# Performance work log

Hardware: AMD Instinct MI355X
Metric: run time of the kernel (lower is better)

Reference implementation:

```python
import jax, jax.numpy as jnp
import numpy as np

B, N, H, D, E = 32, 1000, 256, 128, 512000
NB = B * N


def setup_inputs() -> dict:
    key = jax.random.key(0)
    ks = jax.random.split(key, 16)
    s = 0.05
    inp = {
        "x": jax.random.normal(ks[0], (B, D), jnp.float32),
        "h_prev": jax.random.normal(ks[1], (B, N, H), jnp.float32),
        "c_prev": jax.random.normal(ks[2], (B, N, H), jnp.float32),
        "src": jax.random.randint(ks[3], (E,), 0, NB, jnp.int32),
        "dst": jax.random.randint(ks[4], (E,), 0, NB, jnp.int32),
        "Wi": jax.random.normal(ks[5], (D, H), jnp.float32) * s,
        "bi": jax.random.normal(ks[6], (H,), jnp.float32) * s,
        "Wf": jax.random.normal(ks[7], (D, H), jnp.float32) * s,
        "bf": jax.random.normal(ks[8], (H,), jnp.float32) * s,
        "Wo": jax.random.normal(ks[9], (D, H), jnp.float32) * s,
        "bo": jax.random.normal(ks[10], (H,), jnp.float32) * s,
        "Wc": jax.random.normal(ks[11], (D, H), jnp.float32) * s,
        "bc": jax.random.normal(ks[12], (H,), jnp.float32) * s,
        "Wg": jax.random.normal(ks[13], (H, H), jnp.float32) * s,
        "bg": jax.random.normal(ks[14], (H,), jnp.float32) * s,
    }
    return inp


def _graph_conv(src, dst, h, Wg, bg):
    # DGL GraphConv, norm='both': D_dst^{-1/2} * sum_edges (D_src^{-1/2} * h_src) @ W + b
    nb = h.shape[0]
    ones = jnp.ones(src.shape[0], h.dtype)
    deg_out = jnp.maximum(jax.ops.segment_sum(ones, src, num_segments=nb), 1.0)
    deg_in = jnp.maximum(jax.ops.segment_sum(ones, dst, num_segments=nb), 1.0)
    h = h * (deg_out ** -0.5)[:, None]          # pre-normalize by src out-degree
    agg = jax.ops.segment_sum(h[src], dst, num_segments=nb)  # irregular gather/scatter
    agg = agg * (deg_in ** -0.5)[:, None]       # post-normalize by dst in-degree
    return agg @ Wg + bg


def reference(x, h_prev, c_prev, src, dst, Wi, bi, Wf, bf, Wo, bo, Wc, bc, Wg, bg):
    b, n, hh = h_prev.shape
    h_conv = _graph_conv(src, dst, h_prev.reshape(b * n, hh), Wg, bg).reshape(b, n, hh)
    # four input-gate projections, broadcast over nodes
    xi = (x @ Wi + bi)[:, None, :]
    xf = (x @ Wf + bf)[:, None, :]
    xo = (x @ Wo + bo)[:, None, :]
    xc = (x @ Wc + bc)[:, None, :]
    i_t = jax.nn.sigmoid(xi + h_conv)
    f_t = jax.nn.sigmoid(xf + h_conv)
    o_t = jax.nn.sigmoid(xo + h_conv)
    c_tilde = jnp.tanh(xc + h_conv)
    c_t = f_t * c_prev + i_t * c_tilde
    h_t = o_t * jnp.tanh(c_t)
    return h_t, c_t
```

## Files before the change

### kernel.cpp

```cpp
#include <hip/hip_runtime.h>

#define BB 32
#define NN 1000
#define HH 256
#define DD 128
#define EE 512000
#define NB (BB * NN)
#define PADLOG 6
#define PAD (1 << PADLOG)

#define DEGO_OFF 0
#define DEGI_OFF (NB)
#define GATE_OFF (2 * NB)
#define WGB_OFF (GATE_OFF + 4 * BB * HH)
#define PADC_OFF (WGB_OFF + (HH * HH) / 2)
#define HW_OFF (PADC_OFF + NB * PAD)

using bf16x8 = __attribute__((ext_vector_type(8))) short;
using f32x4 = __attribute__((ext_vector_type(4))) float;

__device__ inline unsigned short f2bf(float x) {
    unsigned u = __float_as_uint(x);
    return (unsigned short)((u + 0x7FFFu + ((u >> 16) & 1u)) >> 16);
}
__device__ inline float bf2f(unsigned short u) {
    return __uint_as_float(((unsigned)u) << 16);
}

__global__ __launch_bounds__(256) void k_fatA(
    const int* __restrict__ src, const int* __restrict__ dst,
    int* __restrict__ deg_out, int* __restrict__ deg_in,
    int* __restrict__ padded, const float* __restrict__ Wg,
    unsigned short* __restrict__ wgb, const float* __restrict__ x,
    const float* __restrict__ Wi, const float* __restrict__ bi,
    const float* __restrict__ Wf, const float* __restrict__ bf_,
    const float* __restrict__ Wo, const float* __restrict__ bo,
    const float* __restrict__ Wc, const float* __restrict__ bc,
    float* __restrict__ gates) {
    int blk = blockIdx.x;
    int t = threadIdx.x;
    if (blk < BB) {
        __shared__ float xs[DD];
        int b = blk;
        if (t < DD) xs[t] = x[b * DD + t];
        __syncthreads();
        float ai = bi[t], af = bf_[t], ao = bo[t], ac = bc[t];
#pragma unroll 4
        for (int k = 0; k < DD; k++) {
            float xv = xs[k];
            ai += xv * Wi[k * HH + t];
            af += xv * Wf[k * HH + t];
            ao += xv * Wo[k * HH + t];
            ac += xv * Wc[k * HH + t];
        }
        gates[0 * BB * HH + b * HH + t] = ai;
        gates[1 * BB * HH + b * HH + t] = af;
        gates[2 * BB * HH + b * HH + t] = ao;
        gates[3 * BB * HH + b * HH + t] = ac;
    } else if (blk < BB + 256) {
        int o = (blk - BB) * 256 + t;
        int j = o & 7;
        int c = o >> 3;
        int lane = c & 63;
        int nt = (c >> 6) & 15;
        int kk = c >> 10;
        int k = kk * 32 + (lane >> 4) * 8 + j;
        int n = nt * 16 + (lane & 15);
        wgb[o] = f2bf(Wg[k * HH + n]);
    } else {
        int e = (blk - (BB + 256)) * 256 + t;
        int s = src[e];
        int d = dst[e];
        atomicAdd(&deg_out[s], 1);
        int p = atomicAdd(&deg_in[d], 1);
        if (p < PAD) padded[(d << PADLOG) + p] = s;
    }
}

__global__ __launch_bounds__(256) void k_fatC(
    const int* __restrict__ deg_out, const float* __restrict__ h,
    const unsigned short* __restrict__ wgb, unsigned short* __restrict__ hw) {
    int blk = blockIdx.x;
    int t = threadIdx.x;
    int lane = t & 63;
    int w = t >> 6;
    int quad = lane >> 4;
    int mrow = lane & 15;
    int r0 = blk * 64 + w * 16;
    int row = r0 + mrow;
    float sc = rsqrtf((float)max(deg_out[row], 1));

    f32x4 acc[16];
#pragma unroll
    for (int nt = 0; nt < 16; nt++) acc[nt] = (f32x4){0.f, 0.f, 0.f, 0.f};

#pragma unroll 1
    for (int kk = 0; kk < 8; kk++) {
        const float* ap = h + (size_t)row * HH + kk * 32 + quad * 8;
        float4 a0 = *(const float4*)ap;
        float4 a1 = *(const float4*)(ap + 4);
        bf16x8 af;
        af[0] = (short)f2bf(a0.x * sc);
        af[1] = (short)f2bf(a0.y * sc);
        af[2] = (short)f2bf(a0.z * sc);
        af[3] = (short)f2bf(a0.w * sc);
        af[4] = (short)f2bf(a1.x * sc);
        af[5] = (short)f2bf(a1.y * sc);
        af[6] = (short)f2bf(a1.z * sc);
        af[7] = (short)f2bf(a1.w * sc);
#pragma unroll
        for (int nt = 0; nt < 16; nt++) {
            bf16x8 bfr =
                *(const bf16x8*)(wgb + (((kk * 16 + nt) * 64 + lane) << 3));
            acc[nt] = __builtin_amdgcn_mfma_f32_16x16x32_bf16(af, bfr, acc[nt],
                                                              0, 0, 0);
        }
    }
#pragma unroll
    for (int nt = 0; nt < 16; nt++) {
#pragma unroll
        for (int reg = 0; reg < 4; reg++) {
            hw[(size_t)(r0 + quad * 4 + reg) * HH + nt * 16 + mrow] =
                f2bf(acc[nt][reg]);
        }
    }
}

__device__ inline void lstm1(float hc, float gi, float gf, float go, float gc,
                             float cp, float& ho, float& co) {
    float pi = gi + hc, pf = gf + hc, po = go + hc, pc = gc + hc;
    float it = 1.f / (1.f + __expf(-pi));
    float ft = 1.f / (1.f + __expf(-pf));
    float ot = 1.f / (1.f + __expf(-po));
    float e2 = __expf(2.f * pc);
    float ctl = (e2 - 1.f) / (e2 + 1.f);
    float ct = ft * cp + it * ctl;
    float e2c = __expf(2.f * ct);
    ho = ot * (e2c - 1.f) / (e2c + 1.f);
    co = ct;
}

__global__ __launch_bounds__(256) void k_out(
    const unsigned short* __restrict__ hw, const int* __restrict__ padded,
    const int* __restrict__ deg_in, const float* __restrict__ bg,
    const float* __restrict__ gates, const float* __restrict__ c_prev,
    float* __restrict__ h_out, float* __restrict__ c_out) {
    int t = threadIdx.x;
    int lane = t & 63;
    int w = t >> 6;
    int node = blockIdx.x * 4 + w;
    int dcnt = deg_in[node];
    float si = rsqrtf((float)max(dcnt, 1));
    int cnt = min(dcnt, PAD);
    int beg = node << PADLOG;
    int end = beg + cnt;
    int col = lane * 4;
    const unsigned short* hwc = hw + col;

    float ax = 0.f, ay = 0.f, az = 0.f, aw = 0.f;
    int e = beg;
    for (; e + 8 <= end; e += 8) {
        int s0 = padded[e + 0];
        int s1 = padded[e + 1];
        int s2 = padded[e + 2];
        int s3 = padded[e + 3];
        int s4 = padded[e + 4];
        int s5 = padded[e + 5];
        int s6 = padded[e + 6];
        int s7 = padded[e + 7];
        ushort4 q0 = *(const ushort4*)(hwc + ((size_t)s0 << 8));
        ushort4 q1 = *(const ushort4*)(hwc + ((size_t)s1 << 8));
        ushort4 q2 = *(const ushort4*)(hwc + ((size_t)s2 << 8));
        ushort4 q3 = *(const ushort4*)(hwc + ((size_t)s3 << 8));
        ushort4 q4 = *(const ushort4*)(hwc + ((size_t)s4 << 8));
        ushort4 q5 = *(const ushort4*)(hwc + ((size_t)s5 << 8));
        ushort4 q6 = *(const ushort4*)(hwc + ((size_t)s6 << 8));
        ushort4 q7 = *(const ushort4*)(hwc + ((size_t)s7 << 8));
        ax += ((bf2f(q0.x) + bf2f(q1.x)) + (bf2f(q2.x) + bf2f(q3.x))) +
              ((bf2f(q4.x) + bf2f(q5.x)) + (bf2f(q6.x) + bf2f(q7.x)));
        ay += ((bf2f(q0.y) + bf2f(q1.y)) + (bf2f(q2.y) + bf2f(q3.y))) +
              ((bf2f(q4.y) + bf2f(q5.y)) + (bf2f(q6.y) + bf2f(q7.y)));
        az += ((bf2f(q0.z) + bf2f(q1.z)) + (bf2f(q2.z) + bf2f(q3.z))) +
              ((bf2f(q4.z) + bf2f(q5.z)) + (bf2f(q6.z) + bf2f(q7.z)));
        aw += ((bf2f(q0.w) + bf2f(q1.w)) + (bf2f(q2.w) + bf2f(q3.w))) +
              ((bf2f(q4.w) + bf2f(q5.w)) + (bf2f(q6.w) + bf2f(q7.w)));
    }
    for (; e + 4 <= end; e += 4) {
        int s0 = padded[e + 0];
        int s1 = padded[e + 1];
        int s2 = padded[e + 2];
        int s3 = padded[e + 3];
        ushort4 q0 = *(const ushort4*)(hwc + ((size_t)s0 << 8));
        ushort4 q1 = *(const ushort4*)(hwc + ((size_t)s1 << 8));
        ushort4 q2 = *(const ushort4*)(hwc + ((size_t)s2 << 8));
        ushort4 q3 = *(const ushort4*)(hwc + ((size_t)s3 << 8));
        ax += (bf2f(q0.x) + bf2f(q1.x)) + (bf2f(q2.x) + bf2f(q3.x));
        ay += (bf2f(q0.y) + bf2f(q1.y)) + (bf2f(q2.y) + bf2f(q3.y));
        az += (bf2f(q0.z) + bf2f(q1.z)) + (bf2f(q2.z) + bf2f(q3.z));
        aw += (bf2f(q0.w) + bf2f(q1.w)) + (bf2f(q2.w) + bf2f(q3.w));
    }
    for (; e < end; e++) {
        int s = padded[e];
        ushort4 q = *(const ushort4*)(hwc + ((size_t)s << 8));
        ax += bf2f(q.x);
        ay += bf2f(q.y);
        az += bf2f(q.z);
        aw += bf2f(q.w);
    }

    int b = node / NN;
    float4 bgv = *(const float4*)(bg + col);
    float4 gi = *(const float4*)(gates + 0 * BB * HH + b * HH + col);
    float4 gf = *(const float4*)(gates + 1 * BB * HH + b * HH + col);
    float4 go = *(const float4*)(gates + 2 * BB * HH + b * HH + col);
    float4 gc = *(const float4*)(gates + 3 * BB * HH + b * HH + col);
    float4 cp = *(const float4*)(c_prev + (size_t)node * HH + col);

    float4 ho, co;
    lstm1(ax * si + bgv.x, gi.x, gf.x, go.x, gc.x, cp.x, ho.x, co.x);
    lstm1(ay * si + bgv.y, gi.y, gf.y, go.y, gc.y, cp.y, ho.y, co.y);
    lstm1(az * si + bgv.z, gi.z, gf.z, go.z, gc.z, cp.z, ho.z, co.z);
    lstm1(aw * si + bgv.w, gi.w, gf.w, go.w, gc.w, cp.w, ho.w, co.w);

    *(float4*)(h_out + (size_t)node * HH + col) = ho;
    *(float4*)(c_out + (size_t)node * HH + col) = co;
}

extern "C" void kernel_launch(void* const* d_in, const int* in_sizes, int n_in,
                              void* d_out, int out_size, void* d_ws,
                              size_t ws_size, hipStream_t stream) {
    const float* x = (const float*)d_in[0];
    const float* h_prev = (const float*)d_in[1];
    const float* c_prev = (const float*)d_in[2];
    const int* src = (const int*)d_in[3];
    const int* dst = (const int*)d_in[4];
    const float* Wi = (const float*)d_in[5];
    const float* bi = (const float*)d_in[6];
    const float* Wf = (const float*)d_in[7];
    const float* bf_ = (const float*)d_in[8];
    const float* Wo = (const float*)d_in[9];
    const float* bo = (const float*)d_in[10];
    const float* Wc = (const float*)d_in[11];
    const float* bc = (const float*)d_in[12];
    const float* Wg = (const float*)d_in[13];
    const float* bg = (const float*)d_in[14];

    int* wsi = (int*)d_ws;
    float* wsf = (float*)d_ws;
    int* deg_out = wsi + DEGO_OFF;
    int* deg_in = wsi + DEGI_OFF;
    float* gates = wsf + GATE_OFF;
    unsigned short* wgb = (unsigned short*)(wsi + WGB_OFF);
    int* padded = wsi + PADC_OFF;
    unsigned short* hw = (unsigned short*)(wsi + HW_OFF);
    float* h_out = (float*)d_out;
    float* c_out = h_out + (size_t)NB * HH;

    hipMemsetAsync(deg_out, 0, (size_t)2 * NB * 4, stream);

    k_fatA<<<BB + 256 + EE / 256, 256, 0, stream>>>(
        src, dst, deg_out, deg_in, padded, Wg, wgb, x, Wi, bi, Wf, bf_, Wo,
        bo, Wc, bc, gates);
    k_fatC<<<NB / 64, 256, 0, stream>>>(deg_out, h_prev, wgb, hw);
    k_out<<<NB / 4, 256, 0, stream>>>(hw, padded, deg_in, bg, gates, c_prev,
                                      h_out, c_out);
}
```

Measured before the change: 268.6 us.

## Move src-degree scaling to gather and overlap edge counting with GEMM

The per-source out-degree normalization is moved from the pre-GEMM scaling of h into the gather loop, where each neighbor row is weighted by rsqrt(deg_out[s]). This removes the dependency between edge counting and the h@Wg MFMA GEMM, so both now run as blocks of one fused launch. The hipMemsetAsync is replaced by zeroing inside the first kernel, and the 4-wide gather tail loop is dropped. The cost is an extra deg_out lookup and rsqrt per gathered edge, and the GEMM blocks now share the GPU with atomic-heavy edge blocks.

Result: faster. 257.1 us (-4.3%).

```diff
diff --git a/kernel.cpp b/kernel.cpp
--- a/kernel.cpp
+++ b/kernel.cpp
@@ -27,16 +27,14 @@
     return __uint_as_float(((unsigned)u) << 16);
 }
 
-__global__ __launch_bounds__(256) void k_fatA(
-    const int* __restrict__ src, const int* __restrict__ dst,
+__global__ __launch_bounds__(256) void k_pre(
     int* __restrict__ deg_out, int* __restrict__ deg_in,
-    int* __restrict__ padded, const float* __restrict__ Wg,
-    unsigned short* __restrict__ wgb, const float* __restrict__ x,
-    const float* __restrict__ Wi, const float* __restrict__ bi,
-    const float* __restrict__ Wf, const float* __restrict__ bf_,
-    const float* __restrict__ Wo, const float* __restrict__ bo,
-    const float* __restrict__ Wc, const float* __restrict__ bc,
-    float* __restrict__ gates) {
+    const float* __restrict__ Wg, unsigned short* __restrict__ wgb,
+    const float* __restrict__ x, const float* __restrict__ Wi,
+    const float* __restrict__ bi, const float* __restrict__ Wf,
+    const float* __restrict__ bf_, const float* __restrict__ Wo,
+    const float* __restrict__ bo, const float* __restrict__ Wc,
+    const float* __restrict__ bc, float* __restrict__ gates) {
     int blk = blockIdx.x;
     int t = threadIdx.x;
     if (blk < BB) {
@@ -68,61 +66,69 @@
         int n = nt * 16 + (lane & 15);
         wgb[o] = f2bf(Wg[k * HH + n]);
     } else {
-        int e = (blk - (BB + 256)) * 256 + t;
+        int idx = (blk - (BB + 256)) * 256 + t;
+        deg_out[idx] = 0;
+        deg_in[idx] = 0;
+    }
+}
+
+__global__ __launch_bounds__(256) void k_mid(
+    const int* __restrict__ src, const int* __restrict__ dst,
+    int* __restrict__ deg_out, int* __restrict__ deg_in,
+    int* __restrict__ padded, const float* __restrict__ h,
+    const unsigned short* __restrict__ wgb, unsigned short* __restrict__ hw) {
+    int blk = blockIdx.x;
+    if (blk < NB / 64) {
+        int t = threadIdx.x;
+        int lane = t & 63;
+        int w = t >> 6;
+        int quad = lane >> 4;
+        int mrow = lane & 15;
+        int r0 = blk * 64 + w * 16;
+        int row = r0 + mrow;
+
+        f32x4 acc[16];
+#pragma unroll
+        for (int nt = 0; nt < 16; nt++) acc[nt] = (f32x4){0.f, 0.f, 0.f, 0.f};
+
+#pragma unroll 1
+        for (int kk = 0; kk < 8; kk++) {
+            const float* ap = h + (size_t)row * HH + kk * 32 + quad * 8;
+            float4 a0 = *(const float4*)ap;
+            float4 a1 = *(const float4*)(ap + 4);
+            bf16x8 af;
+            af[0] = (short)f2bf(a0.x);
+            af[1] = (short)f2bf(a0.y);
+            af[2] = (short)f2bf(a0.z);
+            af[3] = (short)f2bf(a0.w);
+            af[4] = (short)f2bf(a1.x);
+            af[5] = (short)f2bf(a1.y);
+            af[6] = (short)f2bf(a1.z);
+            af[7] = (short)f2bf(a1.w);
+#pragma unroll
+            for (int nt = 0; nt < 16; nt++) {
+                bf16x8 bfr =
+                    *(const bf16x8*)(wgb + (((kk * 16 + nt) * 64 + lane) << 3));
+                acc[nt] = __builtin_amdgcn_mfma_f32_16x16x32_bf16(af, bfr,
+                                                                  acc[nt], 0,
+                                                                  0, 0);
+            }
+        }
+#pragma unroll
+        for (int nt = 0; nt < 16; nt++) {
+#pragma unroll
+            for (int reg = 0; reg < 4; reg++) {
+                hw[(size_t)(r0 + quad * 4 + reg) * HH + nt * 16 + mrow] =
+                    f2bf(acc[nt][reg]);
+            }
+        }
+    } else {
+        int e = (blk - NB / 64) * 256 + threadIdx.x;
         int s = src[e];
         int d = dst[e];
         atomicAdd(&deg_out[s], 1);
         int p = atomicAdd(&deg_in[d], 1);
         if (p < PAD) padded[(d << PADLOG) + p] = s;
-    }
-}
-
-__global__ __launch_bounds__(256) void k_fatC(
-    const int* __restrict__ deg_out, const float* __restrict__ h,
-    const unsigned short* __restrict__ wgb, unsigned short* __restrict__ hw) {
-    int blk = blockIdx.x;
-    int t = threadIdx.x;
-    int lane = t & 63;
-    int w = t >> 6;
-    int quad = lane >> 4;
-    int mrow = lane & 15;
-    int r0 = blk * 64 + w * 16;
-    int row = r0 + mrow;
-    float sc = rsqrtf((float)max(deg_out[row], 1));
-
-    f32x4 acc[16];
-#pragma unroll
-    for (int nt = 0; nt < 16; nt++) acc[nt] = (f32x4){0.f, 0.f, 0.f, 0.f};
-
-#pragma unroll 1
-    for (int kk = 0; kk < 8; kk++) {
-        const float* ap = h + (size_t)row * HH + kk * 32 + quad * 8;
-        float4 a0 = *(const float4*)ap;
-        float4 a1 = *(const float4*)(ap + 4);
-        bf16x8 af;
-        af[0] = (short)f2bf(a0.x * sc);
-        af[1] = (short)f2bf(a0.y * sc);
-        af[2] = (short)f2bf(a0.z * sc);
-        af[3] = (short)f2bf(a0.w * sc);
-        af[4] = (short)f2bf(a1.x * sc);
-        af[5] = (short)f2bf(a1.y * sc);
-        af[6] = (short)f2bf(a1.z * sc);
-        af[7] = (short)f2bf(a1.w * sc);
-#pragma unroll
-        for (int nt = 0; nt < 16; nt++) {
-            bf16x8 bfr =
-                *(const bf16x8*)(wgb + (((kk * 16 + nt) * 64 + lane) << 3));
-            acc[nt] = __builtin_amdgcn_mfma_f32_16x16x32_bf16(af, bfr, acc[nt],
-                                                              0, 0, 0);
-        }
-    }
-#pragma unroll
-    for (int nt = 0; nt < 16; nt++) {
-#pragma unroll
-        for (int reg = 0; reg < 4; reg++) {
-            hw[(size_t)(r0 + quad * 4 + reg) * HH + nt * 16 + mrow] =
-                f2bf(acc[nt][reg]);
-        }
     }
 }
 
@@ -142,9 +148,10 @@
 
 __global__ __launch_bounds__(256) void k_out(
     const unsigned short* __restrict__ hw, const int* __restrict__ padded,
-    const int* __restrict__ deg_in, const float* __restrict__ bg,
-    const float* __restrict__ gates, const float* __restrict__ c_prev,
-    float* __restrict__ h_out, float* __restrict__ c_out) {
+    const int* __restrict__ deg_in, const int* __restrict__ deg_out,
+    const float* __restrict__ bg, const float* __restrict__ gates,
+    const float* __restrict__ c_prev, float* __restrict__ h_out,
+    float* __restrict__ c_out) {
     int t = threadIdx.x;
     int lane = t & 63;
     int w = t >> 6;
@@ -168,6 +175,14 @@
         int s5 = padded[e + 5];
         int s6 = padded[e + 6];
         int s7 = padded[e + 7];
+        float c0 = rsqrtf((float)max(deg_out[s0], 1));
+        float c1 = rsqrtf((float)max(deg_out[s1], 1));
+        float c2 = rsqrtf((float)max(deg_out[s2], 1));
+        float c3 = rsqrtf((float)max(deg_out[s3], 1));
+        float c4 = rsqrtf((float)max(deg_out[s4], 1));
+        float c5 = rsqrtf((float)max(deg_out[s5], 1));
+        float c6 = rsqrtf((float)max(deg_out[s6], 1));
+        float c7 = rsqrtf((float)max(deg_out[s7], 1));
         ushort4 q0 = *(const ushort4*)(hwc + ((size_t)s0 << 8));
         ushort4 q1 = *(const ushort4*)(hwc + ((size_t)s1 << 8));
         ushort4 q2 = *(const ushort4*)(hwc + ((size_t)s2 << 8));
@@ -176,36 +191,31 @@
         ushort4 q5 = *(const ushort4*)(hwc + ((size_t)s5 << 8));
         ushort4 q6 = *(const ushort4*)(hwc + ((size_t)s6 << 8));
         ushort4 q7 = *(const ushort4*)(hwc + ((size_t)s7 << 8));
-        ax += ((bf2f(q0.x) + bf2f(q1.x)) + (bf2f(q2.x) + bf2f(q3.x))) +
-              ((bf2f(q4.x) + bf2f(q5.x)) + (bf2f(q6.x) + bf2f(q7.x)));
-        ay += ((bf2f(q0.y) + bf2f(q1.y)) + (bf2f(q2.y) + bf2f(q3.y))) +
-              ((bf2f(q4.y) + bf2f(q5.y)) + (bf2f(q6.y) + bf2f(q7.y)));
-        az += ((bf2f(q0.z) + bf2f(q1.z)) + (bf2f(q2.z) + bf2f(q3.z))) +
-              ((bf2f(q4.z) + bf2f(q5.z)) + (bf2f(q6.z) + bf2f(q7.z)));
-        aw += ((bf2f(q0.w) + bf2f(q1.w)) + (bf2f(q2.w) + bf2f(q3.w))) +
-              ((bf2f(q4.w) + bf2f(q5.w)) + (bf2f(q6.w) + bf2f(q7.w)));
-    }
-    for (; e + 4 <= end; e += 4) {
-        int s0 = padded[e + 0];
-        int s1 = padded[e + 1];
-        int s2 = padded[e + 2];
-        int s3 = padded[e + 3];
-        ushort4 q0 = *(const ushort4*)(hwc + ((size_t)s0 << 8));
-        ushort4 q1 = *(const ushort4*)(hwc + ((size_t)s1 << 8));
-        ushort4 q2 = *(const ushort4*)(hwc + ((size_t)s2 << 8));
-        ushort4 q3 = *(const ushort4*)(hwc + ((size_t)s3 << 8));
-        ax += (bf2f(q0.x) + bf2f(q1.x)) + (bf2f(q2.x) + bf2f(q3.x));
-        ay += (bf2f(q0.y) + bf2f(q1.y)) + (bf2f(q2.y) + bf2f(q3.y));
-        az += (bf2f(q0.z) + bf2f(q1.z)) + (bf2f(q2.z) + bf2f(q3.z));
-        aw += (bf2f(q0.w) + bf2f(q1.w)) + (bf2f(q2.w) + bf2f(q3.w));
+        ax += ((c0 * bf2f(q0.x) + c1 * bf2f(q1.x)) +
+               (c2 * bf2f(q2.x) + c3 * bf2f(q3.x))) +
+              ((c4 * bf2f(q4.x) + c5 * bf2f(q5.x)) +
+               (c6 * bf2f(q6.x) + c7 * bf2f(q7.x)));
+        ay += ((c0 * bf2f(q0.y) + c1 * bf2f(q1.y)) +
+               (c2 * bf2f(q2.y) + c3 * bf2f(q3.y))) +
+              ((c4 * bf2f(q4.y) + c5 * bf2f(q5.y)) +
+               (c6 * bf2f(q6.y) + c7 * bf2f(q7.y)));
+        az += ((c0 * bf2f(q0.z) + c1 * bf2f(q1.z)) +
+               (c2 * bf2f(q2.z) + c3 * bf2f(q3.z))) +
+              ((c4 * bf2f(q4.z) + c5 * bf2f(q5.z)) +
+               (c6 * bf2f(q6.z) + c7 * bf2f(q7.z)));
+        aw += ((c0 * bf2f(q0.w) + c1 * bf2f(q1.w)) +
+               (c2 * bf2f(q2.w) + c3 * bf2f(q3.w))) +
+              ((c4 * bf2f(q4.w) + c5 * bf2f(q5.w)) +
+               (c6 * bf2f(q6.w) + c7 * bf2f(q7.w)));
     }
     for (; e < end; e++) {
         int s = padded[e];
+        float cc = rsqrtf((float)max(deg_out[s], 1));
         ushort4 q = *(const ushort4*)(hwc + ((size_t)s << 8));
-        ax += bf2f(q.x);
-        ay += bf2f(q.y);
-        az += bf2f(q.z);
-        aw += bf2f(q.w);
+        ax += cc * bf2f(q.x);
+        ay += cc * bf2f(q.y);
+        az += cc * bf2f(q.z);
+        aw += cc * bf2f(q.w);
     }
 
     int b = node / NN;
@@ -256,12 +266,10 @@
     float* h_out = (float*)d_out;
     float* c_out = h_out + (size_t)NB * HH;
 
-    hipMemsetAsync(deg_out, 0, (size_t)2 * NB * 4, stream);
-
-    k_fatA<<<BB + 256 + EE / 256, 256, 0, stream>>>(
-        src, dst, deg_out, deg_in, padded, Wg, wgb, x, Wi, bi, Wf, bf_, Wo,
-        bo, Wc, bc, gates);
-    k_fatC<<<NB / 64, 256, 0, stream>>>(deg_out, h_prev, wgb, hw);
-    k_out<<<NB / 4, 256, 0, stream>>>(hw, padded, deg_in, bg, gates, c_prev,
-                                      h_out, c_out);
-}
+    k_pre<<<BB + 256 + NB / 256, 256, 0, stream>>>(
+        deg_out, deg_in, Wg, wgb, x, Wi, bi, Wf, bf_, Wo, bo, Wc, bc, gates);
+    k_mid<<<NB / 64 + EE / 256, 256, 0, stream>>>(src, dst, deg_out, deg_in,
+                                                  padded, h_prev, wgb, hw);
+    k_out<<<NB / 4, 256, 0, stream>>>(hw, padded, deg_in, deg_out, bg, gates,
+                                      c_prev, h_out, c_out);
+}
```
